# Performance work log

Measured on AMD Instinct MI355X. Metric: run time of the kernel, lower is better.

## Reference

```python
import jax, jax.numpy as jnp
import numpy as np

B, F, U, G = 2048, 512, 512, 64
REG_STRENGTH = 1.0


def setup_inputs() -> dict:
    key = jax.random.key(0)
    k0, k1, k2, k3, k4 = jax.random.split(key, 5)
    x = jax.random.normal(k0, (B, F), dtype=jnp.float32)
    gid = jax.random.randint(k1, (B,), 0, G, dtype=jnp.int64)
    # glorot-normal-ish scale for kernels: sqrt(2/(fan_in+fan_out))
    glorot = np.sqrt(2.0 / (U + F)).astype(np.float32)
    w_mu = jax.random.normal(k2, (G, U, F), dtype=jnp.float32) * glorot
    b_mu = jax.random.normal(k3, (G, U), dtype=jnp.float32) * 0.05  # 'random_normal' init
    w0_mu = jax.random.normal(k4, (U, F), dtype=jnp.float32) * glorot
    b0_mu = jnp.zeros((U,), dtype=jnp.float32)
    return {"x": x, "gid": gid, "w_mu": w_mu, "b_mu": b_mu, "w0_mu": w0_mu, "b0_mu": b0_mu}


def reference(x, gid, w_mu, b_mu, w0_mu, b0_mu):
    # Hard top-1 routing: per-sample weight matrix gather, [B, U, F]
    w = jnp.take(w_mu, gid, axis=0)
    b = jnp.take(b_mu, gid, axis=0)  # [B, U]
    # Batched matvec: 'Bup,Bp->Bu'
    outputs = jnp.einsum("buf,bf->bu", w, x) + b  # use_bias=True, activation=None
    # L2 prior regularization loss (added via add_loss in the original)
    w_loss = jnp.sum(jnp.square(w - w0_mu[None]))  # sum over axes [1,2] then batch
    b_loss = jnp.sum(jnp.square(b - b0_mu[None]))
    reg_loss = REG_STRENGTH * (w_loss + b_loss)
    return outputs, reg_loss
```

## Files before the change

### kernel.cpp

```cpp
#include <hip/hip_runtime.h>

#define B_SZ 2048
#define F_SZ 512
#define U_SZ 512
#define G_SZ 64
#define REG_STRENGTH 1.0f

#define THREADS 256
#define NBLOCKS 512
#define MC 64
#define BK 64
#define NSTEP (F_SZ / BK)

typedef float f32x4 __attribute__((ext_vector_type(4)));
typedef __bf16 bf16x8 __attribute__((ext_vector_type(8)));

#define MFMA(a, b, c) __builtin_amdgcn_mfma_f32_16x16x32_bf16((a), (b), (c), 0, 0, 0)

static __device__ __forceinline__ void split4(const f32x4 v, ushort4* h,
                                              ushort4* l) {
  unsigned short hb[4], lb[4];
#pragma unroll
  for (int i = 0; i < 4; ++i) {
    const __bf16 t = (__bf16)v[i];
    hb[i] = __builtin_bit_cast(unsigned short, t);
    lb[i] = __builtin_bit_cast(unsigned short, (__bf16)(v[i] - (float)t));
  }
  *h = make_ushort4(hb[0], hb[1], hb[2], hb[3]);
  *l = make_ushort4(lb[0], lb[1], lb[2], lb[3]);
}

__global__ __launch_bounds__(1024) void prep_kernel(
    const int* __restrict__ gid, int* __restrict__ counts,
    int* __restrict__ rowstart, int* __restrict__ order) {
  __shared__ int cnt_s[G_SZ];
  __shared__ int cur_s[G_SZ];
  const int tid = threadIdx.x;

  if (tid < G_SZ) cnt_s[tid] = 0;
  __syncthreads();

  for (int b = tid; b < B_SZ; b += 1024) atomicAdd(&cnt_s[gid[b]], 1);
  __syncthreads();

  if (tid == 0) {
    int run = 0;
    for (int g = 0; g < G_SZ; ++g) { cur_s[g] = run; run += cnt_s[g]; }
  }
  __syncthreads();

  if (tid < G_SZ) { counts[tid] = cnt_s[tid]; rowstart[tid] = cur_s[tid]; }
  __syncthreads();

  for (int b = tid; b < B_SZ; b += 1024) {
    int pos = atomicAdd(&cur_s[gid[b]], 1);
    order[pos] = b;
  }
}

__global__ __launch_bounds__(THREADS, 2) void gemm_kernel(
    const float* __restrict__ x, const float* __restrict__ w_mu,
    const float* __restrict__ b_mu, const float* __restrict__ w0_mu,
    const float* __restrict__ b0_mu, float* __restrict__ out,
    float* __restrict__ wsf, unsigned* __restrict__ done,
    const int* __restrict__ counts, const int* __restrict__ rowstart,
    const int* __restrict__ order) {
  __shared__ __align__(16) unsigned short WH[2][MC * BK];
  __shared__ __align__(16) unsigned short WL[2][MC * BK];
  __shared__ __align__(16) unsigned short XH[2][MC * BK];
  __shared__ __align__(16) unsigned short XL[2][MC * BK];
  __shared__ float red_s[4];

  const int bid = blockIdx.x;
  const int g = bid & 63;
  const int nt = bid >> 6;
  const int n0 = nt << 6;

  const int tid = threadIdx.x;
  const int lane = tid & 63;
  const int wv = tid >> 6;
  const int llo = lane & 15;
  const int lhi = lane >> 4;

  const int srow = tid >> 4;
  const int kq = tid & 15;

  const int cnt = counts[g];

  if (cnt > 0) {
    const int rs = rowstart[g];
    const int mycol = n0 + (wv << 4) + llo;
    const float* __restrict__ wgp =
        w_mu + ((size_t)g << 18) + (size_t)(n0 + srow) * F_SZ + (kq << 2);
    const float* __restrict__ w0p =
        w0_mu + (size_t)(n0 + srow) * F_SZ + (kq << 2);

    float regp = 0.0f;
    if (nt == 0) {
#pragma unroll
      for (int u = 0; u < 2; ++u) {
        const int idx = (u << 8) + tid;
        const float d = b_mu[(g << 9) + idx] - b0_mu[idx];
        regp += d * d;
      }
    }

    for (int mc = 0; mc < cnt; mc += MC) {
      const int rc = min(MC, cnt - mc);
      const int mts = (rc + 15) >> 4;
      const bool doreg = (mc == 0);

      const float* xp[4];
#pragma unroll
      for (int u = 0; u < 4; ++u) {
        int sl = mc + srow + (u << 4);
        if (sl >= cnt) sl = cnt - 1;
        xp[u] = x + (size_t)order[rs + sl] * F_SZ + (kq << 2);
      }

      f32x4 acc[4];
#pragma unroll
      for (int m = 0; m < 4; ++m) acc[m] = (f32x4){0.f, 0.f, 0.f, 0.f};

      f32x4 wr[4], xr[4];
#pragma unroll
      for (int u = 0; u < 4; ++u) wr[u] = *(const f32x4*)(wgp + (u << 13));
#pragma unroll
      for (int u = 0; u < 4; ++u) xr[u] = *(const f32x4*)(xp[u]);
      if (doreg) {
#pragma unroll
        for (int u = 0; u < 4; ++u) {
          const f32x4 z = *(const f32x4*)(w0p + (u << 13));
#pragma unroll
          for (int i = 0; i < 4; ++i) {
            const float d = wr[u][i] - z[i];
            regp += d * d;
          }
        }
      }
#pragma unroll
      for (int u = 0; u < 4; ++u) {
        const int row = srow + (u << 4);
        int byte = (row << 7) + (kq << 3);
        byte ^= (row & 7) << 4;
        ushort4 h, l;
        split4(wr[u], &h, &l);
        *(ushort4*)((char*)&WH[0][0] + byte) = h;
        *(ushort4*)((char*)&WL[0][0] + byte) = l;
        split4(xr[u], &h, &l);
        *(ushort4*)((char*)&XH[0][0] + byte) = h;
        *(ushort4*)((char*)&XL[0][0] + byte) = l;
      }
      __syncthreads();

#pragma unroll 2
      for (int s = 0; s < NSTEP; ++s) {
        const int p = s & 1;
        if (s + 1 < NSTEP) {
          const int ko = (s + 1) << 6;
#pragma unroll
          for (int u = 0; u < 4; ++u)
            wr[u] = *(const f32x4*)(wgp + (u << 13) + ko);
#pragma unroll
          for (int u = 0; u < 4; ++u) xr[u] = *(const f32x4*)(xp[u] + ko);
        }
#pragma unroll
        for (int kk = 0; kk < 2; ++kk) {
          const int wrow = (wv << 4) + llo;
          int wb = (wrow << 7) + (kk << 6) + (lhi << 4);
          wb ^= (wrow & 7) << 4;
          const bf16x8 wh = *(const bf16x8*)((const char*)&WH[p][0] + wb);
          const bf16x8 wl = *(const bf16x8*)((const char*)&WL[p][0] + wb);
#pragma unroll
          for (int m = 0; m < 4; ++m) {
            if (m < mts) {
              const int ar = (m << 4) + llo;
              int ab = (ar << 7) + (kk << 6) + (lhi << 4);
              ab ^= (ar & 7) << 4;
              const bf16x8 ah = *(const bf16x8*)((const char*)&XH[p][0] + ab);
              const bf16x8 al = *(const bf16x8*)((const char*)&XL[p][0] + ab);
              acc[m] = MFMA(ah, wh, acc[m]);
              acc[m] = MFMA(ah, wl, acc[m]);
              acc[m] = MFMA(al, wh, acc[m]);
            }
          }
        }
        if (s + 1 < NSTEP) {
          if (doreg) {
            const int ko = (s + 1) << 6;
#pragma unroll
            for (int u = 0; u < 4; ++u) {
              const f32x4 z = *(const f32x4*)(w0p + (u << 13) + ko);
#pragma unroll
              for (int i = 0; i < 4; ++i) {
                const float d = wr[u][i] - z[i];
                regp += d * d;
              }
            }
          }
          const int q = p ^ 1;
#pragma unroll
          for (int u = 0; u < 4; ++u) {
            const int row = srow + (u << 4);
            int byte = (row << 7) + (kq << 3);
            byte ^= (row & 7) << 4;
            ushort4 h, l;
            split4(wr[u], &h, &l);
            *(ushort4*)((char*)&WH[q][0] + byte) = h;
            *(ushort4*)((char*)&WL[q][0] + byte) = l;
            split4(xr[u], &h, &l);
            *(ushort4*)((char*)&XH[q][0] + byte) = h;
            *(ushort4*)((char*)&XL[q][0] + byte) = l;
          }
        }
        __syncthreads();
      }

      const float bias = b_mu[(g << 9) + mycol];
#pragma unroll
      for (int m = 0; m < 4; ++m) {
        if (m < mts) {
#pragma unroll
          for (int j = 0; j < 4; ++j) {
            const int slot = mc + (m << 4) + (lhi << 2) + j;
            if (slot < cnt) {
              out[(size_t)order[rs + slot] * U_SZ + mycol] = acc[m][j] + bias;
            }
          }
        }
      }
    }

#pragma unroll
    for (int o = 32; o > 0; o >>= 1) regp += __shfl_down(regp, o, 64);
    if (lane == 0) red_s[wv] = regp;
    __syncthreads();
    if (tid == 0)
      atomicAdd(wsf, (float)cnt * (red_s[0] + red_s[1] + red_s[2] + red_s[3]));
  }

  if (tid == 0) {
    __threadfence();
    if (atomicAdd(done, 1u) == (unsigned)(NBLOCKS - 1)) {
      const float v = atomicAdd(wsf, 0.0f);
      out[(size_t)B_SZ * U_SZ] = REG_STRENGTH * v;
    }
  }
}

extern "C" void kernel_launch(void* const* d_in, const int* in_sizes, int n_in,
                              void* d_out, int out_size, void* d_ws,
                              size_t ws_size, hipStream_t stream) {
  (void)in_sizes; (void)n_in; (void)out_size; (void)ws_size;
  const float* x     = (const float*)d_in[0];
  const int*   gid   = (const int*)d_in[1];
  const float* w_mu  = (const float*)d_in[2];
  const float* b_mu  = (const float*)d_in[3];
  const float* w0_mu = (const float*)d_in[4];
  const float* b0_mu = (const float*)d_in[5];

  float*    wsf      = (float*)d_ws;
  unsigned* done     = (unsigned*)d_ws + 1;
  int*      counts   = (int*)d_ws + 2;
  int*      rowstart = (int*)d_ws + 2 + G_SZ;
  int*      order    = (int*)d_ws + 2 + 2 * G_SZ;

  hipMemsetAsync(d_ws, 0, 8, stream);
  prep_kernel<<<1, 1024, 0, stream>>>(gid, counts, rowstart, order);
  gemm_kernel<<<NBLOCKS, THREADS, 0, stream>>>(
      x, w_mu, b_mu, w0_mu, b0_mu, (float*)d_out, wsf, done,
      counts, rowstart, order);
}
```

Baseline: 133.9 us.

## Deepen global prefetch to two stages and fold workspace reset into prep

The GEMM K-loop now keeps two register stages of W, x and w0 loads in flight, issuing loads two steps ahead, and writes the next LDS buffer before the MFMAs on the current one. Barriers become an explicit lgkmcnt wait plus s_barrier. The reg-loss path is specialised through a template so later chunks carry no w0 branch. The hipMemsetAsync is removed by zeroing the accumulators inside prep_kernel, and the prefix sum there uses wave shuffles instead of a serial loop. Tripling the in-flight register buffers raises VGPR pressure and may cost occupancy under launch_bounds(256,2).

Measured after the change: 186.5 us. 39.2% more time.

```diff
diff --git a/kernel.cpp b/kernel.cpp
--- a/kernel.cpp
+++ b/kernel.cpp
@@ -17,6 +17,9 @@
 
 #define MFMA(a, b, c) __builtin_amdgcn_mfma_f32_16x16x32_bf16((a), (b), (c), 0, 0, 0)
 
+#define BARRIER_LGKM() \
+  asm volatile("s_waitcnt lgkmcnt(0)\n\ts_barrier" ::: "memory")
+
 static __device__ __forceinline__ void split4(const f32x4 v, ushort4* h,
                                               ushort4* l) {
   unsigned short hb[4], lb[4];
@@ -30,31 +33,185 @@
   *l = make_ushort4(lb[0], lb[1], lb[2], lb[3]);
 }
 
+static __device__ __forceinline__ void stage4(unsigned short* __restrict__ H,
+                                              unsigned short* __restrict__ L,
+                                              int row, int kq, const f32x4 v) {
+  int byte = (row << 7) + (kq << 3);
+  byte ^= (row & 7) << 4;
+  ushort4 h, l;
+  split4(v, &h, &l);
+  *(ushort4*)((char*)H + byte) = h;
+  *(ushort4*)((char*)L + byte) = l;
+}
+
 __global__ __launch_bounds__(1024) void prep_kernel(
     const int* __restrict__ gid, int* __restrict__ counts,
-    int* __restrict__ rowstart, int* __restrict__ order) {
+    int* __restrict__ rowstart, int* __restrict__ order,
+    float* __restrict__ wsf, unsigned* __restrict__ done) {
   __shared__ int cnt_s[G_SZ];
   __shared__ int cur_s[G_SZ];
   const int tid = threadIdx.x;
 
   if (tid < G_SZ) cnt_s[tid] = 0;
+  if (tid == 0) { wsf[0] = 0.0f; *done = 0u; }
   __syncthreads();
 
   for (int b = tid; b < B_SZ; b += 1024) atomicAdd(&cnt_s[gid[b]], 1);
   __syncthreads();
 
-  if (tid == 0) {
-    int run = 0;
-    for (int g = 0; g < G_SZ; ++g) { cur_s[g] = run; run += cnt_s[g]; }
-  }
-  __syncthreads();
-
-  if (tid < G_SZ) { counts[tid] = cnt_s[tid]; rowstart[tid] = cur_s[tid]; }
+  if (tid < G_SZ) {
+    const int c = cnt_s[tid];
+    int inc = c;
+#pragma unroll
+    for (int o = 1; o < G_SZ; o <<= 1) {
+      const int t = __shfl_up(inc, o, 64);
+      if (tid >= o) inc += t;
+    }
+    counts[tid] = c;
+    rowstart[tid] = inc - c;
+    cur_s[tid] = inc - c;
+  }
   __syncthreads();
 
   for (int b = tid; b < B_SZ; b += 1024) {
     int pos = atomicAdd(&cur_s[gid[b]], 1);
     order[pos] = b;
+  }
+}
+
+template <bool DOREG>
+static __device__ __forceinline__ void run_chunk(
+    const float* __restrict__ x, const int* __restrict__ order, int rs,
+    int mc, int cnt, const float* __restrict__ wgp,
+    const float* __restrict__ w0p, unsigned short* __restrict__ WH0,
+    unsigned short* __restrict__ WH1, unsigned short* __restrict__ WL0,
+    unsigned short* __restrict__ WL1, unsigned short* __restrict__ XH0,
+    unsigned short* __restrict__ XH1, unsigned short* __restrict__ XL0,
+    unsigned short* __restrict__ XL1, int srow, int kq, int wv, int llo,
+    int lhi, const float* __restrict__ b_mu, int g, int mycol,
+    float* __restrict__ out, float& regp) {
+  const int rc = min(MC, cnt - mc);
+  const int mts = (rc + 15) >> 4;
+
+  const float* xp[4];
+#pragma unroll
+  for (int u = 0; u < 4; ++u) {
+    int sl = mc + srow + (u << 4);
+    if (sl >= cnt) sl = cnt - 1;
+    xp[u] = x + (size_t)order[rs + sl] * F_SZ + (kq << 2);
+  }
+
+  f32x4 acc[4];
+#pragma unroll
+  for (int m = 0; m < 4; ++m) acc[m] = (f32x4){0.f, 0.f, 0.f, 0.f};
+
+  unsigned short* const WH[2] = {WH0, WH1};
+  unsigned short* const WL[2] = {WL0, WL1};
+  unsigned short* const XH[2] = {XH0, XH1};
+  unsigned short* const XL[2] = {XL0, XL1};
+
+  f32x4 wr[2][4], xr[2][4], zr[2][4];
+#pragma unroll
+  for (int u = 0; u < 4; ++u) wr[0][u] = *(const f32x4*)(wgp + (u << 13));
+#pragma unroll
+  for (int u = 0; u < 4; ++u) xr[0][u] = *(const f32x4*)(xp[u]);
+  if (DOREG) {
+#pragma unroll
+    for (int u = 0; u < 4; ++u) zr[0][u] = *(const f32x4*)(w0p + (u << 13));
+  }
+#pragma unroll
+  for (int u = 0; u < 4; ++u) wr[1][u] = *(const f32x4*)(wgp + (u << 13) + BK);
+#pragma unroll
+  for (int u = 0; u < 4; ++u) xr[1][u] = *(const f32x4*)(xp[u] + BK);
+  if (DOREG) {
+#pragma unroll
+    for (int u = 0; u < 4; ++u)
+      zr[1][u] = *(const f32x4*)(w0p + (u << 13) + BK);
+  }
+
+#pragma unroll
+  for (int u = 0; u < 4; ++u) {
+    const int row = srow + (u << 4);
+    stage4(WH[0], WL[0], row, kq, wr[0][u]);
+    stage4(XH[0], XL[0], row, kq, xr[0][u]);
+    if (DOREG) {
+#pragma unroll
+      for (int i = 0; i < 4; ++i) {
+        const float d = wr[0][u][i] - zr[0][u][i];
+        regp += d * d;
+      }
+    }
+  }
+  BARRIER_LGKM();
+
+#pragma unroll
+  for (int s = 0; s < NSTEP; ++s) {
+    const int cs = s & 1;
+    const int ns = cs ^ 1;
+    if (s + 2 < NSTEP) {
+      const int ko = (s + 2) << 6;
+#pragma unroll
+      for (int u = 0; u < 4; ++u)
+        wr[cs][u] = *(const f32x4*)(wgp + (u << 13) + ko);
+#pragma unroll
+      for (int u = 0; u < 4; ++u) xr[cs][u] = *(const f32x4*)(xp[u] + ko);
+      if (DOREG) {
+#pragma unroll
+        for (int u = 0; u < 4; ++u)
+          zr[cs][u] = *(const f32x4*)(w0p + (u << 13) + ko);
+      }
+    }
+    if (s + 1 < NSTEP) {
+#pragma unroll
+      for (int u = 0; u < 4; ++u) {
+        const int row = srow + (u << 4);
+        stage4(WH[ns], WL[ns], row, kq, wr[ns][u]);
+        stage4(XH[ns], XL[ns], row, kq, xr[ns][u]);
+        if (DOREG) {
+#pragma unroll
+          for (int i = 0; i < 4; ++i) {
+            const float d = wr[ns][u][i] - zr[ns][u][i];
+            regp += d * d;
+          }
+        }
+      }
+    }
+#pragma unroll
+    for (int kk = 0; kk < 2; ++kk) {
+      const int wrow = (wv << 4) + llo;
+      int wb = (wrow << 7) + (kk << 6) + (lhi << 4);
+      wb ^= (wrow & 7) << 4;
+      const bf16x8 wh = *(const bf16x8*)((const char*)WH[cs] + wb);
+      const bf16x8 wl = *(const bf16x8*)((const char*)WL[cs] + wb);
+#pragma unroll
+      for (int m = 0; m < 4; ++m) {
+        if (m < mts) {
+          const int ar = (m << 4) + llo;
+          int ab = (ar << 7) + (kk << 6) + (lhi << 4);
+          ab ^= (ar & 7) << 4;
+          const bf16x8 ah = *(const bf16x8*)((const char*)XH[cs] + ab);
+          const bf16x8 al = *(const bf16x8*)((const char*)XL[cs] + ab);
+          acc[m] = MFMA(ah, wh, acc[m]);
+          acc[m] = MFMA(ah, wl, acc[m]);
+          acc[m] = MFMA(al, wh, acc[m]);
+        }
+      }
+    }
+    BARRIER_LGKM();
+  }
+
+  const float bias = b_mu[(g << 9) + mycol];
+#pragma unroll
+  for (int m = 0; m < 4; ++m) {
+    if (m < mts) {
+#pragma unroll
+      for (int j = 0; j < 4; ++j) {
+        const int slot = mc + (m << 4) + (lhi << 2) + j;
+        if (slot < cnt) {
+          out[(size_t)order[rs + slot] * U_SZ + mycol] = acc[m][j] + bias;
+        }
+      }
+    }
   }
 }
 
@@ -106,128 +263,14 @@
     }
 
     for (int mc = 0; mc < cnt; mc += MC) {
-      const int rc = min(MC, cnt - mc);
-      const int mts = (rc + 15) >> 4;
-      const bool doreg = (mc == 0);
-
-      const float* xp[4];
-#pragma unroll
-      for (int u = 0; u < 4; ++u) {
-        int sl = mc + srow + (u << 4);
-        if (sl >= cnt) sl = cnt - 1;
-        xp[u] = x + (size_t)order[rs + sl] * F_SZ + (kq << 2);
-      }
-
-      f32x4 acc[4];
-#pragma unroll
-      for (int m = 0; m < 4; ++m) acc[m] = (f32x4){0.f, 0.f, 0.f, 0.f};
-
-      f32x4 wr[4], xr[4];
-#pragma unroll
-      for (int u = 0; u < 4; ++u) wr[u] = *(const f32x4*)(wgp + (u << 13));
-#pragma unroll
-      for (int u = 0; u < 4; ++u) xr[u] = *(const f32x4*)(xp[u]);
-      if (doreg) {
-#pragma unroll
-        for (int u = 0; u < 4; ++u) {
-          const f32x4 z = *(const f32x4*)(w0p + (u << 13));
-#pragma unroll
-          for (int i = 0; i < 4; ++i) {
-            const float d = wr[u][i] - z[i];
-            regp += d * d;
-          }
-        }
-      }
-#pragma unroll
-      for (int u = 0; u < 4; ++u) {
-        const int row = srow + (u << 4);
-        int byte = (row << 7) + (kq << 3);
-        byte ^= (row & 7) << 4;
-        ushort4 h, l;
-        split4(wr[u], &h, &l);
-        *(ushort4*)((char*)&WH[0][0] + byte) = h;
-        *(ushort4*)((char*)&WL[0][0] + byte) = l;
-        split4(xr[u], &h, &l);
-        *(ushort4*)((char*)&XH[0][0] + byte) = h;
-        *(ushort4*)((char*)&XL[0][0] + byte) = l;
-      }
-      __syncthreads();
-
-#pragma unroll 2
-      for (int s = 0; s < NSTEP; ++s) {
-        const int p = s & 1;
-        if (s + 1 < NSTEP) {
-          const int ko = (s + 1) << 6;
-#pragma unroll
-          for (int u = 0; u < 4; ++u)
-            wr[u] = *(const f32x4*)(wgp + (u << 13) + ko);
-#pragma unroll
-          for (int u = 0; u < 4; ++u) xr[u] = *(const f32x4*)(xp[u] + ko);
-        }
-#pragma unroll
-        for (int kk = 0; kk < 2; ++kk) {
-          const int wrow = (wv << 4) + llo;
-          int wb = (wrow << 7) + (kk << 6) + (lhi << 4);
-          wb ^= (wrow & 7) << 4;
-          const bf16x8 wh = *(const bf16x8*)((const char*)&WH[p][0] + wb);
-          const bf16x8 wl = *(const bf16x8*)((const char*)&WL[p][0] + wb);
-#pragma unroll
-          for (int m = 0; m < 4; ++m) {
-            if (m < mts) {
-              const int ar = (m << 4) + llo;
-              int ab = (ar << 7) + (kk << 6) + (lhi << 4);
-              ab ^= (ar & 7) << 4;
-              const bf16x8 ah = *(const bf16x8*)((const char*)&XH[p][0] + ab);
-              const bf16x8 al = *(const bf16x8*)((const char*)&XL[p][0] + ab);
-              acc[m] = MFMA(ah, wh, acc[m]);
-              acc[m] = MFMA(ah, wl, acc[m]);
-              acc[m] = MFMA(al, wh, acc[m]);
-            }
-          }
-        }
-        if (s + 1 < NSTEP) {
-          if (doreg) {
-            const int ko = (s + 1) << 6;
-#pragma unroll
-            for (int u = 0; u < 4; ++u) {
-              const f32x4 z = *(const f32x4*)(w0p + (u << 13) + ko);
-#pragma unroll
-              for (int i = 0; i < 4; ++i) {
-                const float d = wr[u][i] - z[i];
-                regp += d * d;
-              }
-            }
-          }
-          const int q = p ^ 1;
-#pragma unroll
-          for (int u = 0; u < 4; ++u) {
-            const int row = srow + (u << 4);
-            int byte = (row << 7) + (kq << 3);
-            byte ^= (row & 7) << 4;
-            ushort4 h, l;
-            split4(wr[u], &h, &l);
-            *(ushort4*)((char*)&WH[q][0] + byte) = h;
-            *(ushort4*)((char*)&WL[q][0] + byte) = l;
-            split4(xr[u], &h, &l);
-            *(ushort4*)((char*)&XH[q][0] + byte) = h;
-            *(ushort4*)((char*)&XL[q][0] + byte) = l;
-          }
-        }
-        __syncthreads();
-      }
-
-      const float bias = b_mu[(g << 9) + mycol];
-#pragma unroll
-      for (int m = 0; m < 4; ++m) {
-        if (m < mts) {
-#pragma unroll
-          for (int j = 0; j < 4; ++j) {
-            const int slot = mc + (m << 4) + (lhi << 2) + j;
-            if (slot < cnt) {
-              out[(size_t)order[rs + slot] * U_SZ + mycol] = acc[m][j] + bias;
-            }
-          }
-        }
+      if (mc == 0) {
+        run_chunk<true>(x, order, rs, 0, cnt, wgp, w0p, WH[0], WH[1], WL[0],
+                        WL[1], XH[0], XH[1], XL[0], XL[1], srow, kq, wv, llo,
+                        lhi, b_mu, g, mycol, out, regp);
+      } else {
+        run_chunk<false>(x, order, rs, mc, cnt, wgp, w0p, WH[0], WH[1], WL[0],
+                         WL[1], XH[0], XH[1], XL[0], XL[1], srow, kq, wv, llo,
+                         lhi, b_mu, g, mycol, out, regp);
       }
     }
 
@@ -265,8 +308,7 @@
   int*      rowstart = (int*)d_ws + 2 + G_SZ;
   int*      order    = (int*)d_ws + 2 + 2 * G_SZ;
 
-  hipMemsetAsync(d_ws, 0, 8, stream);
-  prep_kernel<<<1, 1024, 0, stream>>>(gid, counts, rowstart, order);
+  prep_kernel<<<1, 1024, 0, stream>>>(gid, counts, rowstart, order, wsf, done);
   gemm_kernel<<<NBLOCKS, THREADS, 0, stream>>>(
       x, w_mu, b_mu, w0_mu, b0_mu, (float*)d_out, wsf, done,
       counts, rowstart, order);
```

## Halve column tile, double grid, shrink K step and fold memset into prep

Applied to the files above, without the earlier changes.

The grouped GEMM now uses 32-column tiles per block, which gives 1024 blocks instead of 512, and a 32-wide K step with a new LDS swizzle. Each wave computes two 16-row M fragments for one 16-column half. Launch bounds move to 4 blocks per SM for higher occupancy, and MFMA sections are wrapped in s_setprio. The workspace memset is folded into prep_kernel and the serial prefix sum becomes a wave shuffle scan, which saves one launch. In exchange, x rows are reloaded twice as often across column tiles and there are more barrier steps per K.

Result: slower. 153.9 us (+14.9%).

```diff
diff --git a/kernel.cpp b/kernel.cpp
--- a/kernel.cpp
+++ b/kernel.cpp
@@ -7,9 +7,10 @@
 #define REG_STRENGTH 1.0f
 
 #define THREADS 256
-#define NBLOCKS 512
+#define NCT 16
+#define NBLOCKS (G_SZ * NCT)
 #define MC 64
-#define BK 64
+#define BK 32
 #define NSTEP (F_SZ / BK)
 
 typedef float f32x4 __attribute__((ext_vector_type(4)));
@@ -30,26 +31,50 @@
   *l = make_ushort4(lb[0], lb[1], lb[2], lb[3]);
 }
 
+static __device__ __forceinline__ void stage4(unsigned short* __restrict__ H,
+                                              unsigned short* __restrict__ L,
+                                              int row, int kq, const f32x4 v) {
+  int byte = (row << 6) + (kq << 3);
+  byte ^= ((row >> 1) & 3) << 4;
+  ushort4 h, l;
+  split4(v, &h, &l);
+  *(ushort4*)((char*)H + byte) = h;
+  *(ushort4*)((char*)L + byte) = l;
+}
+
+static __device__ __forceinline__ int fragoff(int row, int lhi) {
+  int byte = (row << 6) + (lhi << 4);
+  byte ^= ((row >> 1) & 3) << 4;
+  return byte;
+}
+
 __global__ __launch_bounds__(1024) void prep_kernel(
     const int* __restrict__ gid, int* __restrict__ counts,
-    int* __restrict__ rowstart, int* __restrict__ order) {
+    int* __restrict__ rowstart, int* __restrict__ order,
+    float* __restrict__ wsf, unsigned* __restrict__ done) {
   __shared__ int cnt_s[G_SZ];
   __shared__ int cur_s[G_SZ];
   const int tid = threadIdx.x;
 
   if (tid < G_SZ) cnt_s[tid] = 0;
+  if (tid == 0) { wsf[0] = 0.0f; *done = 0u; }
   __syncthreads();
 
   for (int b = tid; b < B_SZ; b += 1024) atomicAdd(&cnt_s[gid[b]], 1);
   __syncthreads();
 
-  if (tid == 0) {
-    int run = 0;
-    for (int g = 0; g < G_SZ; ++g) { cur_s[g] = run; run += cnt_s[g]; }
-  }
-  __syncthreads();
-
-  if (tid < G_SZ) { counts[tid] = cnt_s[tid]; rowstart[tid] = cur_s[tid]; }
+  if (tid < G_SZ) {
+    const int c = cnt_s[tid];
+    int inc = c;
+#pragma unroll
+    for (int o = 1; o < G_SZ; o <<= 1) {
+      const int t = __shfl_up(inc, o, 64);
+      if (tid >= o) inc += t;
+    }
+    counts[tid] = c;
+    rowstart[tid] = inc - c;
+    cur_s[tid] = inc - c;
+  }
   __syncthreads();
 
   for (int b = tid; b < B_SZ; b += 1024) {
@@ -58,45 +83,47 @@
   }
 }
 
-__global__ __launch_bounds__(THREADS, 2) void gemm_kernel(
+__global__ __launch_bounds__(THREADS, 4) void gemm_kernel(
     const float* __restrict__ x, const float* __restrict__ w_mu,
     const float* __restrict__ b_mu, const float* __restrict__ w0_mu,
     const float* __restrict__ b0_mu, float* __restrict__ out,
     float* __restrict__ wsf, unsigned* __restrict__ done,
     const int* __restrict__ counts, const int* __restrict__ rowstart,
     const int* __restrict__ order) {
-  __shared__ __align__(16) unsigned short WH[2][MC * BK];
-  __shared__ __align__(16) unsigned short WL[2][MC * BK];
-  __shared__ __align__(16) unsigned short XH[2][MC * BK];
-  __shared__ __align__(16) unsigned short XL[2][MC * BK];
+  __shared__ __align__(16) unsigned short WHs[2][32 * BK];
+  __shared__ __align__(16) unsigned short WLs[2][32 * BK];
+  __shared__ __align__(16) unsigned short XHs[2][MC * BK];
+  __shared__ __align__(16) unsigned short XLs[2][MC * BK];
   __shared__ float red_s[4];
 
   const int bid = blockIdx.x;
   const int g = bid & 63;
-  const int nt = bid >> 6;
-  const int n0 = nt << 6;
+  const int ct = bid >> 6;
+  const int n0 = ct << 5;
 
   const int tid = threadIdx.x;
   const int lane = tid & 63;
   const int wv = tid >> 6;
+  const int mh = wv >> 1;
+  const int chalf = wv & 1;
   const int llo = lane & 15;
   const int lhi = lane >> 4;
 
-  const int srow = tid >> 4;
-  const int kq = tid & 15;
+  const int srow = tid >> 3;
+  const int kq = tid & 7;
 
   const int cnt = counts[g];
 
   if (cnt > 0) {
     const int rs = rowstart[g];
-    const int mycol = n0 + (wv << 4) + llo;
+    const int mycol = n0 + (chalf << 4) + llo;
     const float* __restrict__ wgp =
-        w_mu + ((size_t)g << 18) + (size_t)(n0 + srow) * F_SZ + (kq << 2);
+        w_mu + ((size_t)g << 18) + ((size_t)(n0 + srow) << 9) + (kq << 2);
     const float* __restrict__ w0p =
-        w0_mu + (size_t)(n0 + srow) * F_SZ + (kq << 2);
+        w0_mu + ((size_t)(n0 + srow) << 9) + (kq << 2);
 
     float regp = 0.0f;
-    if (nt == 0) {
+    if (ct == 0) {
 #pragma unroll
       for (int u = 0; u < 2; ++u) {
         const int idx = (u << 8) + tid;
@@ -110,122 +137,105 @@
       const int mts = (rc + 15) >> 4;
       const bool doreg = (mc == 0);
 
-      const float* xp[4];
-#pragma unroll
-      for (int u = 0; u < 4; ++u) {
-        int sl = mc + srow + (u << 4);
-        if (sl >= cnt) sl = cnt - 1;
-        xp[u] = x + (size_t)order[rs + sl] * F_SZ + (kq << 2);
-      }
-
-      f32x4 acc[4];
-#pragma unroll
-      for (int m = 0; m < 4; ++m) acc[m] = (f32x4){0.f, 0.f, 0.f, 0.f};
-
-      f32x4 wr[4], xr[4];
-#pragma unroll
-      for (int u = 0; u < 4; ++u) wr[u] = *(const f32x4*)(wgp + (u << 13));
-#pragma unroll
-      for (int u = 0; u < 4; ++u) xr[u] = *(const f32x4*)(xp[u]);
+      int slA = mc + srow;      if (slA >= cnt) slA = cnt - 1;
+      int slB = mc + 32 + srow; if (slB >= cnt) slB = cnt - 1;
+      const float* __restrict__ xpA =
+          x + ((size_t)order[rs + slA] << 9) + (kq << 2);
+      const float* __restrict__ xpB =
+          x + ((size_t)order[rs + slB] << 9) + (kq << 2);
+
+      f32x4 acc0 = {0.f, 0.f, 0.f, 0.f};
+      f32x4 acc1 = {0.f, 0.f, 0.f, 0.f};
+
+      f32x4 wr = *(const f32x4*)(wgp);
+      f32x4 xrA = *(const f32x4*)(xpA);
+      f32x4 xrB = *(const f32x4*)(xpB);
       if (doreg) {
-#pragma unroll
-        for (int u = 0; u < 4; ++u) {
-          const f32x4 z = *(const f32x4*)(w0p + (u << 13));
-#pragma unroll
-          for (int i = 0; i < 4; ++i) {
-            const float d = wr[u][i] - z[i];
-            regp += d * d;
-          }
-        }
-      }
-#pragma unroll
-      for (int u = 0; u < 4; ++u) {
-        const int row = srow + (u << 4);
-        int byte = (row << 7) + (kq << 3);
-        byte ^= (row & 7) << 4;
-        ushort4 h, l;
-        split4(wr[u], &h, &l);
-        *(ushort4*)((char*)&WH[0][0] + byte) = h;
-        *(ushort4*)((char*)&WL[0][0] + byte) = l;
-        split4(xr[u], &h, &l);
-        *(ushort4*)((char*)&XH[0][0] + byte) = h;
-        *(ushort4*)((char*)&XL[0][0] + byte) = l;
-      }
+        const f32x4 z = *(const f32x4*)(w0p);
+#pragma unroll
+        for (int i = 0; i < 4; ++i) {
+          const float d = wr[i] - z[i];
+          regp += d * d;
+        }
+      }
+      stage4(WHs[0], WLs[0], srow, kq, wr);
+      stage4(XHs[0], XLs[0], srow, kq, xrA);
+      stage4(XHs[0], XLs[0], srow + 32, kq, xrB);
       __syncthreads();
 
 #pragma unroll 2
       for (int s = 0; s < NSTEP; ++s) {
         const int p = s & 1;
         if (s + 1 < NSTEP) {
-          const int ko = (s + 1) << 6;
-#pragma unroll
-          for (int u = 0; u < 4; ++u)
-            wr[u] = *(const f32x4*)(wgp + (u << 13) + ko);
-#pragma unroll
-          for (int u = 0; u < 4; ++u) xr[u] = *(const f32x4*)(xp[u] + ko);
-        }
-#pragma unroll
-        for (int kk = 0; kk < 2; ++kk) {
-          const int wrow = (wv << 4) + llo;
-          int wb = (wrow << 7) + (kk << 6) + (lhi << 4);
-          wb ^= (wrow & 7) << 4;
-          const bf16x8 wh = *(const bf16x8*)((const char*)&WH[p][0] + wb);
-          const bf16x8 wl = *(const bf16x8*)((const char*)&WL[p][0] + wb);
-#pragma unroll
-          for (int m = 0; m < 4; ++m) {
-            if (m < mts) {
-              const int ar = (m << 4) + llo;
-              int ab = (ar << 7) + (kk << 6) + (lhi << 4);
-              ab ^= (ar & 7) << 4;
-              const bf16x8 ah = *(const bf16x8*)((const char*)&XH[p][0] + ab);
-              const bf16x8 al = *(const bf16x8*)((const char*)&XL[p][0] + ab);
-              acc[m] = MFMA(ah, wh, acc[m]);
-              acc[m] = MFMA(ah, wl, acc[m]);
-              acc[m] = MFMA(al, wh, acc[m]);
-            }
-          }
-        }
+          const int ko = (s + 1) << 5;
+          wr = *(const f32x4*)(wgp + ko);
+          xrA = *(const f32x4*)(xpA + ko);
+          xrB = *(const f32x4*)(xpB + ko);
+        }
+        __builtin_amdgcn_s_setprio(1);
+        {
+          const int wrow = (chalf << 4) + llo;
+          const bf16x8 wh =
+              *(const bf16x8*)((const char*)WHs[p] + fragoff(wrow, lhi));
+          const bf16x8 wl =
+              *(const bf16x8*)((const char*)WLs[p] + fragoff(wrow, lhi));
+          const int m0 = mh << 1;
+          if (m0 < mts) {
+            const int ar = (m0 << 4) + llo;
+            const bf16x8 ah =
+                *(const bf16x8*)((const char*)XHs[p] + fragoff(ar, lhi));
+            const bf16x8 al =
+                *(const bf16x8*)((const char*)XLs[p] + fragoff(ar, lhi));
+            acc0 = MFMA(ah, wh, acc0);
+            acc0 = MFMA(ah, wl, acc0);
+            acc0 = MFMA(al, wh, acc0);
+          }
+          if (m0 + 1 < mts) {
+            const int ar = ((m0 + 1) << 4) + llo;
+            const bf16x8 ah =
+                *(const bf16x8*)((const char*)XHs[p] + fragoff(ar, lhi));
+            const bf16x8 al =
+                *(const bf16x8*)((const char*)XLs[p] + fragoff(ar, lhi));
+            acc1 = MFMA(ah, wh, acc1);
+            acc1 = MFMA(ah, wl, acc1);
+            acc1 = MFMA(al, wh, acc1);
+          }
+        }
+        __builtin_amdgcn_s_setprio(0);
         if (s + 1 < NSTEP) {
           if (doreg) {
-            const int ko = (s + 1) << 6;
-#pragma unroll
-            for (int u = 0; u < 4; ++u) {
-              const f32x4 z = *(const f32x4*)(w0p + (u << 13) + ko);
-#pragma unroll
-              for (int i = 0; i < 4; ++i) {
-                const float d = wr[u][i] - z[i];
-                regp += d * d;
-              }
+            const f32x4 z = *(const f32x4*)(w0p + ((s + 1) << 5));
+#pragma unroll
+            for (int i = 0; i < 4; ++i) {
+              const float d = wr[i] - z[i];
+              regp += d * d;
             }
           }
           const int q = p ^ 1;
-#pragma unroll
-          for (int u = 0; u < 4; ++u) {
-            const int row = srow + (u << 4);
-            int byte = (row << 7) + (kq << 3);
-            byte ^= (row & 7) << 4;
-            ushort4 h, l;
-            split4(wr[u], &h, &l);
-            *(ushort4*)((char*)&WH[q][0] + byte) = h;
-            *(ushort4*)((char*)&WL[q][0] + byte) = l;
-            split4(xr[u], &h, &l);
-            *(ushort4*)((char*)&XH[q][0] + byte) = h;
-            *(ushort4*)((char*)&XL[q][0] + byte) = l;
-          }
+          stage4(WHs[q], WLs[q], srow, kq, wr);
+          stage4(XHs[q], XLs[q], srow, kq, xrA);
+          stage4(XHs[q], XLs[q], srow + 32, kq, xrB);
         }
         __syncthreads();
       }
 
       const float bias = b_mu[(g << 9) + mycol];
-#pragma unroll
-      for (int m = 0; m < 4; ++m) {
-        if (m < mts) {
-#pragma unroll
-          for (int j = 0; j < 4; ++j) {
-            const int slot = mc + (m << 4) + (lhi << 2) + j;
-            if (slot < cnt) {
-              out[(size_t)order[rs + slot] * U_SZ + mycol] = acc[m][j] + bias;
-            }
+      const int m0 = mh << 1;
+      if (m0 < mts) {
+#pragma unroll
+        for (int j = 0; j < 4; ++j) {
+          const int slot = mc + (m0 << 4) + (lhi << 2) + j;
+          if (slot < cnt) {
+            out[(size_t)order[rs + slot] * U_SZ + mycol] = acc0[j] + bias;
+          }
+        }
+      }
+      if (m0 + 1 < mts) {
+#pragma unroll
+        for (int j = 0; j < 4; ++j) {
+          const int slot = mc + ((m0 + 1) << 4) + (lhi << 2) + j;
+          if (slot < cnt) {
+            out[(size_t)order[rs + slot] * U_SZ + mycol] = acc1[j] + bias;
           }
         }
       }
@@ -265,8 +275,7 @@
   int*      rowstart = (int*)d_ws + 2 + G_SZ;
   int*      order    = (int*)d_ws + 2 + 2 * G_SZ;
 
-  hipMemsetAsync(d_ws, 0, 8, stream);
-  prep_kernel<<<1, 1024, 0, stream>>>(gid, counts, rowstart, order);
+  prep_kernel<<<1, 1024, 0, stream>>>(gid, counts, rowstart, order, wsf, done);
   gemm_kernel<<<NBLOCKS, THREADS, 0, stream>>>(
       x, w_mu, b_mu, w0_mu, b0_mu, (float*)d_out, wsf, done,
       counts, rowstart, order);
```
